# Kernel optimization log

Measured on AMD Instinct MI355X. Metric: run time of the kernel, lower is better.

The kernel has to match this reference:

```python
import jax, jax.numpy as jnp
from jax import lax
import numpy as np


def conv2d(x, w, b=None, stride=1, padding=0, groups=1, dilation=1):
    out = lax.conv_general_dilated(
        x, w, (stride, stride), [(padding, padding)] * 2,
        rhs_dilation=(dilation, dilation), feature_group_count=groups,
        dimension_numbers=('NCHW', 'OIHW', 'NCHW'))
    return out if b is None else out + b[None, :, None, None]


def unfold1d(x, k, axis):
    # torch.nn.functional.unfold with kernel (k,1) or (1,k), pad k//2 on that axis.
    # Returns [B, C, k, H, W] (channel-major, kernel-tap inner), matching torch layout.
    pad = k // 2
    pads = [(0, 0)] * 4
    pads[axis] = (pad, pad)
    xp = jnp.pad(x, pads)
    return jnp.stack([lax.slice_in_dim(xp, i, i + x.shape[axis], axis=axis)
                      for i in range(k)], axis=2)


def ikba(x, att, k, g, b_cb, w_cb):
    # Per-pixel dynamic grouped conv: attention mixes nset codebook kernels,
    # applied as vertical (k,1) then horizontal (1,k) unfold-matmul-fold.
    B, c, H, W = x.shape
    nset = att.shape[1]
    cg = c // g
    P = H * W
    a = att.reshape(B, nset, P).transpose(0, 2, 1)          # [B,P,nset]
    bias = a @ b_cb[0]                                      # [B,P,c]
    attk = a @ w_cb[0]                                      # [B,P, 2*c*cg*k]
    half = attk.shape[-1] // 2
    ah = attk[..., :half].reshape(B, P, g, cg, cg * k)
    aw = attk[..., half:].reshape(B, P, g, cg, cg * k)
    # vertical pass
    ufh = unfold1d(x, k, 2).reshape(B, g, cg * k, P).transpose(0, 3, 1, 2)  # [B,P,g,cg*k]
    xh = jnp.einsum('bpgij,bpgj->bpgi', ah, ufh).reshape(B, P, c)
    xh = xh.transpose(0, 2, 1).reshape(B, c, H, W)
    # horizontal pass
    ufw = unfold1d(xh, k, 3).reshape(B, g, cg * k, P).transpose(0, 3, 1, 2)
    xw = jnp.einsum('bpgij,bpgj->bpgi', aw, ufw).reshape(B, P, c) + bias
    return xw.transpose(0, 2, 1).reshape(B, c, H, W)


def hff_forward(x, dw1_w, dw2_w, proj_w, lka0_w, lkas_w, lka1_w, lka1_b,
                sca_w, sca_b, c1a_w, c1b_w, c2a_w, c2a_b, c2b_w, c2b_b,
                c211_w, c211_b, w_cb, b_cb, attgamma, ga1):
    C = x.shape[1]
    K, GC = 3, 4
    g = C // GC
    sca = conv2d(jnp.mean(x, axis=(2, 3), keepdims=True), sca_w, sca_b)
    x1 = conv2d(conv2d(x, dw1_w), dw2_w, padding=1, groups=C)
    lka = conv2d(conv2d(conv2d(x, lka0_w, padding=2, groups=C),
                        lkas_w, padding=9, groups=C, dilation=3), lka1_w, lka1_b)
    t = conv2d(x, c2a_w, c2a_b, padding=1, groups=c2a_w.shape[0])
    t1, t2 = jnp.split(t, 2, axis=1)  # SimpleGate
    att = conv2d(t1 * t2, c2b_w, c2b_b) * attgamma + conv2d(x, c211_w, c211_b)
    uf = conv2d(conv2d(x, c1a_w), c1b_w, padding=1, groups=C)
    x2 = ikba(uf, att, K, g, b_cb, w_cb) * ga1 + uf
    return conv2d(x1 * x2 * sca * lka, proj_w)


def setup_inputs() -> dict:
    key = jax.random.key(0)
    ks = jax.random.split(key, 24)
    B, C, H, W = 2, 256, 64, 64
    nset, k, gc = 128, 3, 4
    g = C // gc
    cg = C // g
    def rn(i, shape, scale=0.02):
        return jax.random.normal(ks[i], shape, jnp.float32) * scale
    return {
        'x': jax.random.normal(ks[0], (B, C, H, W), jnp.float32),
        'dw1_w': rn(1, (C, C, 1, 1)),
        'dw2_w': rn(2, (C, 1, 3, 3), 0.1),
        'proj_w': rn(3, (C, C, 1, 1)),
        'lka0_w': rn(4, (C, 1, 5, 5), 0.1),
        'lkas_w': rn(5, (C, 1, 7, 7), 0.1),
        'lka1_w': rn(6, (C, C, 1, 1)),
        'lka1_b': rn(7, (C,)),
        'sca_w': rn(8, (C, C, 1, 1)),
        'sca_b': rn(9, (C,)),
        'c1a_w': rn(10, (C, C, 1, 1)),
        'c1b_w': rn(11, (C, 1, 3, 3), 0.1),
        'c2a_w': rn(12, (32, C // 32, 3, 3), 0.1),
        'c2a_b': rn(13, (32,)),
        'c2b_w': rn(14, (nset, 16, 1, 1), 0.1),
        'c2b_b': rn(15, (nset,)),
        'c211_w': rn(16, (nset, C, 1, 1)),
        'c211_b': rn(17, (nset,)),
        'w_cb': rn(18, (1, nset, C * cg * k * 2), 0.05),
        'b_cb': rn(19, (1, nset, C), 0.05),
        'attgamma': jnp.full((1, nset, 1, 1), 0.01, jnp.float32),
        'ga1': jnp.full((1, C, 1, 1), 0.01, jnp.float32),
    }


def reference(x, dw1_w, dw2_w, proj_w, lka0_w, lkas_w, lka1_w, lka1_b,
              sca_w, sca_b, c1a_w, c1b_w, c2a_w, c2a_b, c2b_w, c2b_b,
              c211_w, c211_b, w_cb, b_cb, attgamma, ga1):
    return hff_forward(x, dw1_w, dw2_w, proj_w, lka0_w, lkas_w, lka1_w, lka1_b,
                       sca_w, sca_b, c1a_w, c1b_w, c2a_w, c2a_b, c2b_w, c2b_b,
                       c211_w, c211_b, w_cb, b_cb, attgamma, ga1)
```

## Files before the change

### kernel.cpp

```cpp
#include <hip/hip_runtime.h>
#include <cstddef>

#define P_ 4096
#define HW_ 64

typedef __bf16 bf16x8 __attribute__((ext_vector_type(8)));
typedef float f32x4 __attribute__((ext_vector_type(4)));

__device__ inline ushort f2bf(float f) {
  unsigned u = __float_as_uint(f);
  unsigned r = (u + 0x7FFFu + ((u >> 16) & 1u)) >> 16;
  return (ushort)r;
}
__device__ inline float bf2f(ushort h) {
  return __uint_as_float(((unsigned)h) << 16);
}
__device__ inline unsigned pack2(ushort a, ushort b) {
  return (unsigned)a | ((unsigned)b << 16);
}


__device__ inline void xsplit_body(const float* sb, ushort* dhb, ushort* dlb,
                                   int p0, int K, char* smem) {
  float (*T)[65] = (float(*)[65])smem;
  int t = threadIdx.x;
#pragma unroll
  for (int i = 0; i < 32; ++i) {
    int l = i * 256 + t;
    int n = l >> 6, c = l & 63;
    T[n][c] = sb[(size_t)n * P_ + p0 + c];
  }
  __syncthreads();
#pragma unroll
  for (int i = 0; i < 4; ++i) {
    int l = i * 256 + t;
    int c = l >> 4, n8 = (l & 15) << 3;
    ushort vh[8], vl[8];
#pragma unroll
    for (int u = 0; u < 8; ++u) {
      float f = T[n8 + u][c];
      ushort h = f2bf(f);
      vh[u] = h;
      vl[u] = f2bf(f - bf2f(h));
    }
    *(uint4*)&dhb[(size_t)(p0 + c) * K + n8] = *(uint4*)vh;
    *(uint4*)&dlb[(size_t)(p0 + c) * K + n8] = *(uint4*)vl;
  }
}

__device__ inline void gemm_body(const ushort* Whb, const ushort* Wlb,
                                 const ushort* Xhb, const ushort* Xlb,
                                 const float* bias, float* out, int M, int m0,
                                 int p0, int b, int K, char* smem) {
  ushort* Wsh = (ushort*)smem;
  ushort* Wsl = (ushort*)(smem + 9216);
  ushort* Xsh = (ushort*)(smem + 18432);
  ushort* Xsl = (ushort*)(smem + 27648);
  int t = threadIdx.x;
  int w = t >> 6, lane = t & 63, lm = lane & 15, lq = lane >> 4;
  f32x4 C[4];
#pragma unroll
  for (int pt = 0; pt < 4; ++pt) C[pt] = (f32x4)(0.f);
  for (int k0 = 0; k0 < K; k0 += 64) {
#pragma unroll
    for (int i = 0; i < 2; ++i) {
      int u = i * 256 + t;
      int row = u >> 3, k8 = (u & 7) * 8;
      *(uint4*)&Wsh[row * 72 + k8] = *(const uint4*)&Whb[(size_t)row * K + k0 + k8];
      *(uint4*)&Wsl[row * 72 + k8] = *(const uint4*)&Wlb[(size_t)row * K + k0 + k8];
      *(uint4*)&Xsh[row * 72 + k8] = *(const uint4*)&Xhb[(size_t)row * K + k0 + k8];
      *(uint4*)&Xsl[row * 72 + k8] = *(const uint4*)&Xlb[(size_t)row * K + k0 + k8];
    }
    __syncthreads();
#pragma unroll
    for (int kt = 0; kt < 2; ++kt) {
      bf16x8 Ah = *(const bf16x8*)&Wsh[(w * 16 + lm) * 72 + kt * 32 + lq * 8];
      bf16x8 Al = *(const bf16x8*)&Wsl[(w * 16 + lm) * 72 + kt * 32 + lq * 8];
#pragma unroll
      for (int pt = 0; pt < 4; ++pt) {
        bf16x8 Bh = *(const bf16x8*)&Xsh[(pt * 16 + lm) * 72 + kt * 32 + lq * 8];
        bf16x8 Bl = *(const bf16x8*)&Xsl[(pt * 16 + lm) * 72 + kt * 32 + lq * 8];
        C[pt] = __builtin_amdgcn_mfma_f32_16x16x32_bf16(Ah, Bh, C[pt], 0, 0, 0);
        C[pt] = __builtin_amdgcn_mfma_f32_16x16x32_bf16(Al, Bh, C[pt], 0, 0, 0);
        C[pt] = __builtin_amdgcn_mfma_f32_16x16x32_bf16(Ah, Bl, C[pt], 0, 0, 0);
      }
    }
    __syncthreads();
  }
#pragma unroll
  for (int pt = 0; pt < 4; ++pt) {
    int p = p0 + pt * 16 + lm;
#pragma unroll
    for (int r = 0; r < 4; ++r) {
      int m = m0 + w * 16 + lq * 4 + r;
      float v = C[pt][r];
      if (bias) v += bias[m];
      out[((size_t)b * M + m) * P_ + p] = v;
    }
  }
}

__global__ __launch_bounds__(256) void prep_kernel(
    const float* __restrict__ w_cb, const float* __restrict__ dw1_w,
    const float* __restrict__ lka1_w, const float* __restrict__ c1a_w,
    const float* __restrict__ proj_w, const float* __restrict__ c211_w,
    const float* __restrict__ b_cb, ushort* __restrict__ wT,
    ushort* __restrict__ W5h, ushort* __restrict__ W5l,
    ushort* __restrict__ bth, ushort* __restrict__ btl,
    const float* __restrict__ x, float* __restrict__ mean,
    ushort* __restrict__ XTxh, ushort* __restrict__ XTxl) {
  __shared__ __align__(16) char smem[33280];
  float (*T)[65] = (float(*)[65])smem;
  int blk = blockIdx.x;
  int t = threadIdx.x;
  if (blk < 96) {
    int c0 = blk * 64;
#pragma unroll
    for (int i = 0; i < 32; ++i) {
      int l = i * 256 + t;
      int n = l >> 6, c = l & 63;
      T[n][c] = w_cb[(size_t)n * 6144 + c0 + c];
    }
    __syncthreads();
#pragma unroll
    for (int i = 0; i < 4; ++i) {
      int l = i * 256 + t;
      int c = l >> 4, n8 = (l & 15) << 3;
      ushort v[8];
#pragma unroll
      for (int u = 0; u < 8; ++u) v[u] = f2bf(T[n8 + u][c]);
      *(uint4*)&wT[(size_t)(c0 + c) * 128 + n8] = *(uint4*)v;
    }
  } else if (blk < 240) {
    int f = (blk - 96) * 2048 + t * 8;
    const float* srcs[5] = {dw1_w, lka1_w, c1a_w, proj_w, c211_w};
    const int base[6] = {0, 65536, 131072, 196608, 262144, 294912};
    int r = 0;
    while (f >= base[r + 1]) ++r;
    const float* s = srcs[r] + (f - base[r]);
    float4 a = *(const float4*)s;
    float4 b4 = *(const float4*)(s + 4);
    float vv[8] = {a.x, a.y, a.z, a.w, b4.x, b4.y, b4.z, b4.w};
    ushort vh[8], vl[8];
#pragma unroll
    for (int u = 0; u < 8; ++u) {
      ushort h = f2bf(vv[u]);
      vh[u] = h;
      vl[u] = f2bf(vv[u] - bf2f(h));
    }
    *(uint4*)&W5h[f] = *(uint4*)vh;
    *(uint4*)&W5l[f] = *(uint4*)vl;
  } else if (blk < 244) {
    int c0 = (blk - 240) * 64;
#pragma unroll
    for (int i = 0; i < 32; ++i) {
      int l = i * 256 + t;
      int n = l >> 6, c = l & 63;
      T[n][c] = b_cb[(size_t)n * 256 + c0 + c];
    }
    __syncthreads();
#pragma unroll
    for (int i = 0; i < 4; ++i) {
      int l = i * 256 + t;
      int c = l >> 4, n8 = (l & 15) << 3;
      ushort vh[8], vl[8];
#pragma unroll
      for (int u = 0; u < 8; ++u) {
        float fv = T[n8 + u][c];
        ushort h = f2bf(fv);
        vh[u] = h;
        vl[u] = f2bf(fv - bf2f(h));
      }
      *(uint4*)&bth[(size_t)(c0 + c) * 128 + n8] = *(uint4*)vh;
      *(uint4*)&btl[(size_t)(c0 + c) * 128 + n8] = *(uint4*)vl;
    }
  } else if (blk < 756) {
    int bc = blk - 244;
    const float* xp = x + (size_t)bc * P_;
    float s = 0.f;
    for (int i = t; i < P_; i += 256) s += xp[i];
    float* red = (float*)smem;
    red[t] = s;
    __syncthreads();
    for (int off2 = 128; off2 > 0; off2 >>= 1) {
      if (t < off2) red[t] += red[t + off2];
      __syncthreads();
    }
    if (t == 0) mean[bc] = red[0] * (1.f / P_);
  } else {
    const int K = 256;
    int l = blk - 756;
    int p0 = (l & 63) * 64;
    int kb = (l >> 6) & 1;
    int b = l >> 7;
    xsplit_body(x + ((size_t)b * K + kb * 128) * P_,
                XTxh + (size_t)b * P_ * K + (size_t)kb * 128,
                XTxl + (size_t)b * P_ * K + (size_t)kb * 128, p0, K, smem);
  }
}

__global__ __launch_bounds__(256) void main1_kernel(
    const ushort* __restrict__ Xh, const ushort* __restrict__ Xl,
    const ushort* __restrict__ W5h, const ushort* __restrict__ W5l,
    const float* __restrict__ c211_b, float* __restrict__ B1,
    float* __restrict__ B3, float* __restrict__ att0,
    const float* __restrict__ x, const float* __restrict__ w0,
    const float* __restrict__ w1, float* __restrict__ outlka,
    const float* __restrict__ c2aw, const float* __restrict__ c2ab,
    float* __restrict__ sgate, const float* __restrict__ mean,
    const float* __restrict__ sca_w, const float* __restrict__ sca_b,
    float* __restrict__ sca) {
  __shared__ __align__(16) char smem[48448];
  int blk = blockIdx.x;
  int t = threadIdx.x;
  if (blk < 512) {
    float* p0a = (float*)smem;
    float* p1a = (float*)(smem + 19584);
    int bc = blk;
    const float* ib = x + (size_t)bc * P_;
    const float* wp0 = w0 + (size_t)(bc & 255) * 25;
    const float* wp1 = w1 + (size_t)(bc & 255) * 49;
    for (int i = t; i < 4896; i += 256) p0a[i] = 0.f;
    for (int i = t; i < 7216; i += 256) p1a[i] = 0.f;
    __syncthreads();
#pragma unroll
    for (int i = 0; i < 4; ++i) {
      int l = i * 1024 + t * 4;
      int y = l >> 6, xx = l & 63;
      *(float4*)&p0a[(y + 2) * 72 + 4 + xx] = *(const float4*)(ib + l);
    }
    __syncthreads();
    int x0 = (t & 15) * 4, y0 = (t >> 4) * 4;
    {
      float acc[4][4] = {};
#pragma unroll
      for (int ry = 0; ry < 8; ++ry) {
        const float* row = &p0a[(y0 + ry) * 72 + x0];
        float4 v0 = *(const float4*)row;
        float4 v1 = *(const float4*)(row + 4);
        float4 v2 = *(const float4*)(row + 8);
        float rv[12] = {v0.x, v0.y, v0.z, v0.w, v1.x, v1.y, v1.z, v1.w,
                        v2.x, v2.y, v2.z, v2.w};
#pragma unroll
        for (int oy = 0; oy < 4; ++oy) {
          int dy = ry - oy;
          if (dy >= 0 && dy <= 4) {
#pragma unroll
            for (int dx = 0; dx < 5; ++dx) {
              float wv = wp0[dy * 5 + dx];
#pragma unroll
              for (int ox = 0; ox < 4; ++ox)
                acc[oy][ox] += wv * rv[2 + ox + dx];
            }
          }
        }
      }
#pragma unroll
      for (int oy = 0; oy < 4; ++oy) {
        float4 v = {acc[oy][0], acc[oy][1], acc[oy][2], acc[oy][3]};
        *(float4*)&p1a[(y0 + oy + 9) * 88 + 12 + x0] = v;
      }
    }
    __syncthreads();
    {
      float acc[4][4] = {};
#pragma unroll
      for (int ry = 0; ry < 22; ++ry) {
        const float* row = &p1a[(y0 + ry) * 88 + x0];
        float rv[28];
#pragma unroll
        for (int q = 0; q < 7; ++q)
          *(float4*)&rv[q * 4] = *(const float4*)(row + q * 4);
#pragma unroll
        for (int oy = 0; oy < 4; ++oy) {
          int d = ry - oy;
          if (d >= 0 && d <= 18 && (d % 3) == 0) {
            int dy = d / 3;
#pragma unroll
            for (int dx = 0; dx < 7; ++dx) {
              float wv = wp1[dy * 7 + dx];
#pragma unroll
              for (int ox = 0; ox < 4; ++ox)
                acc[oy][ox] += wv * rv[3 + ox + 3 * dx];
            }
          }
        }
      }
      float* ob = outlka + (size_t)bc * P_;
#pragma unroll
      for (int oy = 0; oy < 4; ++oy) {
        float4 v = {acc[oy][0], acc[oy][1], acc[oy][2], acc[oy][3]};
        *(float4*)&ob[(y0 + oy) * 64 + x0] = v;
      }
    }
  } else if (blk < 1024) {
    int idx = (blk - 512) * 256 + t;
    int xq = idx & 63, y = (idx >> 6) & 63, go = (idx >> 12) & 15, b = idx >> 16;
    float acc[2];
#pragma unroll
    for (int h = 0; h < 2; ++h) {
      int gc = go + h * 16;
      const float* wr = c2aw + gc * 72;
      const float* xb = x + ((size_t)b * 256 + gc * 8) * P_;
      float ss = c2ab[gc];
      for (int ci = 0; ci < 8; ++ci)
        for (int dy = 0; dy < 3; ++dy) {
          int yy = y + dy - 1;
          if (yy < 0 || yy >= 64) continue;
          for (int dx = 0; dx < 3; ++dx) {
            int xx = xq + dx - 1;
            if (xx < 0 || xx >= 64) continue;
            ss += wr[ci * 9 + dy * 3 + dx] * xb[(size_t)ci * P_ + yy * 64 + xx];
          }
        }
      acc[h] = ss;
    }
    sgate[idx] = acc[0] * acc[1];
  } else if (blk < 1026) {
    int b = blk - 1024, c = t;
    const float* mb = mean + b * 256;
    const float* wr = sca_w + c * 256;
    float s = sca_b[c];
    for (int k = 0; k < 256; ++k) s += wr[k] * mb[k];
    sca[b * 256 + c] = s;
  } else {
    const int K = 256;
    int g = blk - 1026;
    int p = g & 63;
    int my = (g >> 6) % 10;
    int b = g / 640;
    const ushort *Wh, *Wl;
    float* out;
    const float* bias = nullptr;
    int M, m0;
    if (my < 4) {
      Wh = W5h; Wl = W5l; out = B1; M = 256; m0 = my * 64;
    } else if (my < 8) {
      Wh = W5h + 131072; Wl = W5l + 131072; out = B3; M = 256; m0 = (my - 4) * 64;
    } else {
      Wh = W5h + 262144; Wl = W5l + 262144; out = att0; M = 128;
      m0 = (my - 8) * 64; bias = c211_b;
    }
    int p0 = p * 64;
    gemm_body(Wh + (size_t)m0 * K, Wl + (size_t)m0 * K,
              Xh + ((size_t)b * P_ + p0) * K, Xl + ((size_t)b * P_ + p0) * K,
              bias, out, M, m0, p0, b, K, smem);
  }
}

__global__ __launch_bounds__(256) void dwsplit_kernel(
    const float* __restrict__ in1, const float* __restrict__ w1,
    float* __restrict__ out1, const float* __restrict__ in2,
    const float* __restrict__ w2, float* __restrict__ out2,
    const float* __restrict__ B6, ushort* __restrict__ XT2h,
    ushort* __restrict__ XT2l) {
  __shared__ __align__(16) char smem[33280];
  int blk = blockIdx.x;
  int t = threadIdx.x;
  if (blk < 1024) {
    float* pl = (float*)smem;
    int which = blk >> 9;
    int bc = blk & 511;
    const float* in = which ? in2 : in1;
    const float* w = which ? w2 : w1;
    float* out = which ? out2 : out1;
    const float* ib = in + (size_t)bc * P_;
    const float* wp = w + (size_t)(bc & 255) * 9;
    for (int i = t; i < 4752; i += 256) pl[i] = 0.f;
    __syncthreads();
#pragma unroll
    for (int i = 0; i < 4; ++i) {
      int l = i * 1024 + t * 4;
      int y = l >> 6, xx = l & 63;
      *(float4*)&pl[(y + 1) * 72 + 4 + xx] = *(const float4*)(ib + l);
    }
    __syncthreads();
    int x0 = (t & 15) * 4, y0 = (t >> 4) * 4;
    float acc[4][4] = {};
#pragma unroll
    for (int ry = 0; ry < 6; ++ry) {
      const float* row = &pl[(y0 + ry) * 72 + x0];
      float4 v0 = *(const float4*)row;
      float4 v1 = *(const float4*)(row + 4);
      float4 v2 = *(const float4*)(row + 8);
      float rv[12] = {v0.x, v0.y, v0.z, v0.w, v1.x, v1.y, v1.z, v1.w,
                      v2.x, v2.y, v2.z, v2.w};
#pragma unroll
      for (int oy = 0; oy < 4; ++oy) {
        int dy = ry - oy;
        if (dy >= 0 && dy <= 2) {
#pragma unroll
          for (int dx = 0; dx < 3; ++dx) {
            float wv = wp[dy * 3 + dx];
#pragma unroll
            for (int ox = 0; ox < 4; ++ox)
              acc[oy][ox] += wv * rv[3 + ox + dx];
          }
        }
      }
    }
    float* ob = out + (size_t)bc * P_;
#pragma unroll
    for (int oy = 0; oy < 4; ++oy) {
      float4 v = {acc[oy][0], acc[oy][1], acc[oy][2], acc[oy][3]};
      *(float4*)&ob[(y0 + oy) * 64 + x0] = v;
    }
  } else {
    const int K = 256;
    int l = blk - 1024;
    int p0 = (l & 63) * 64;
    int kb = (l >> 6) & 1;
    int b = l >> 7;
    xsplit_body(B6 + ((size_t)b * K + kb * 128) * P_,
                XT2h + (size_t)b * P_ * K + (size_t)kb * 128,
                XT2l + (size_t)b * P_ * K + (size_t)kb * 128, p0, K, smem);
  }
}

__global__ __launch_bounds__(256) void gemm_c2b_kernel(
    const ushort* __restrict__ Wh, const ushort* __restrict__ Wl,
    const ushort* __restrict__ XT2h, const ushort* __restrict__ XT2l,
    const float* __restrict__ lka1_b, float* __restrict__ B1,
    const float* __restrict__ sb, const float* __restrict__ c2bw,
    const float* __restrict__ c2bb, const float* __restrict__ gamma,
    const float* __restrict__ res, ushort* __restrict__ outh,
    ushort* __restrict__ outl) {
  __shared__ __align__(16) char smem[36864];
  int my = blockIdx.y;
  int b = blockIdx.z;
  int t = threadIdx.x;
  if (my < 4) {
    const int K = 256;
    int p0 = blockIdx.x * 64, m0 = my * 64;
    gemm_body(Wh + (size_t)m0 * K, Wl + (size_t)m0 * K,
              XT2h + ((size_t)b * P_ + p0) * K, XT2l + ((size_t)b * P_ + p0) * K,
              lka1_b, B1, 256, m0, p0, b, K, smem);
  } else {
    const int K = 16, M = 128;
    int p0 = blockIdx.x * 64;
    int m0 = (my - 4) * 64;
    float (*Ws)[68] = (float(*)[68])smem;
    float (*Xs)[68] = (float(*)[68])(smem + 4352 * 4);
    int tm = t >> 4, tp = t & 15;
    float acc[4][4] = {};
    const float* inb = sb + (size_t)b * K * P_;
    {
      int kk = t >> 4, pq = (t & 15) << 2;
      float4 v = *(const float4*)(inb + (size_t)kk * P_ + p0 + pq);
      *(float4*)&Xs[kk][pq] = v;
    }
    {
      int mm = t >> 2, kq = (t & 3) << 2;
      float4 v = *(const float4*)(c2bw + (size_t)(m0 + mm) * K + kq);
      Ws[kq + 0][mm] = v.x; Ws[kq + 1][mm] = v.y;
      Ws[kq + 2][mm] = v.z; Ws[kq + 3][mm] = v.w;
    }
    __syncthreads();
#pragma unroll
    for (int kk = 0; kk < 16; ++kk) {
      const float4 wv = *(const float4*)&Ws[kk][tm << 2];
      const float4 xv = *(const float4*)&Xs[kk][tp << 2];
      const float wa[4] = {wv.x, wv.y, wv.z, wv.w};
      const float xa[4] = {xv.x, xv.y, xv.z, xv.w};
#pragma unroll
      for (int i = 0; i < 4; ++i)
#pragma unroll
        for (int j = 0; j < 4; ++j) acc[i][j] += wa[i] * xa[j];
    }
    float val[4][4];
#pragma unroll
    for (int i = 0; i < 4; ++i) {
      int m = m0 + (tm << 2) + i;
      float bv = c2bb[m], gm = gamma[m];
      float4 rv = *(const float4*)(res + ((size_t)b * M + m) * P_ + p0 + (tp << 2));
      val[i][0] = (acc[i][0] + bv) * gm + rv.x;
      val[i][1] = (acc[i][1] + bv) * gm + rv.y;
      val[i][2] = (acc[i][2] + bv) * gm + rv.z;
      val[i][3] = (acc[i][3] + bv) * gm + rv.w;
    }
#pragma unroll
    for (int j = 0; j < 4; ++j) {
      int p = p0 + (tp << 2) + j;
      ushort vh[4], vl[4];
#pragma unroll
      for (int i = 0; i < 4; ++i) {
        float f = val[i][j];
        ushort h = f2bf(f);
        vh[i] = h;
        vl[i] = f2bf(f - bf2f(h));
      }
      size_t a = ((size_t)b * P_ + p) * 128 + m0 + (tm << 2);
      uint2 hv, lv;
      hv.x = pack2(vh[0], vh[1]); hv.y = pack2(vh[2], vh[3]);
      lv.x = pack2(vl[0], vl[1]); lv.y = pack2(vl[2], vl[3]);
      *(uint2*)&outh[a] = hv;
      *(uint2*)&outl[a] = lv;
    }
  }
}

__global__ __launch_bounds__(256) void ikba_mfma_kernel(
    const float* __restrict__ in, const ushort* __restrict__ attT,
    const ushort* __restrict__ Wt, int dirH, int wofs,
    const ushort* __restrict__ bth, const ushort* __restrict__ btl,
    const float* __restrict__ uf_ep, const float* __restrict__ ga1,
    const float* __restrict__ x1, const float* __restrict__ lka,
    const float* __restrict__ sca, ushort* __restrict__ pXh,
    ushort* __restrict__ pXl, float* __restrict__ outV) {
  __shared__ float Ts[2][4][16][66];
  __shared__ float bls[64 * 17];

  int t = threadIdx.x;
  int b = blockIdx.z;
  int quad = blockIdx.y;
  int y = blockIdx.x;
  int p0 = y * 64;
  int gg = t >> 6;
  int lane = t & 63;
  int lm = lane & 15, lq = lane >> 4;
  int gi = quad * 4 + gg;
  int x = lane;

  const ushort* Wbase = Wt + ((size_t)wofs + (size_t)gi * 48) * 128;
  bf16x8 Af[3][4];
#pragma unroll
  for (int ct = 0; ct < 3; ++ct)
#pragma unroll
    for (int K = 0; K < 4; ++K)
      Af[ct][K] = *(const bf16x8*)&Wbase[(ct * 16 + lm) * 128 + K * 32 + lq * 8];

  const ushort* Ab = attT + ((size_t)b * P_ + p0) * 128;
  f32x4 Cf[3][4];
#pragma unroll
  for (int ct = 0; ct < 3; ++ct)
#pragma unroll
    for (int pt = 0; pt < 4; ++pt) Cf[ct][pt] = (f32x4)(0.f);

#pragma unroll
  for (int pt = 0; pt < 4; ++pt) {
    bf16x8 Bf[4];
#pragma unroll
    for (int K = 0; K < 4; ++K)
      Bf[K] = *(const bf16x8*)&Ab[(pt * 16 + lm) * 128 + K * 32 + lq * 8];
#pragma unroll
    for (int ct = 0; ct < 3; ++ct)
#pragma unroll
      for (int K = 0; K < 4; ++K)
        Cf[ct][pt] = __builtin_amdgcn_mfma_f32_16x16x32_bf16(
            Af[ct][K], Bf[K], Cf[ct][pt], 0, 0, 0);
  }

  if (dirH) {
    f32x4 Cb = (f32x4)(0.f);
#pragma unroll
    for (int K = 0; K < 4; ++K) {
      bf16x8 Bb = *(const bf16x8*)&Ab[(gg * 16 + lm) * 128 + K * 32 + lq * 8];
      bf16x8 Abh = *(const bf16x8*)&bth[(size_t)(quad * 16 + lm) * 128 + K * 32 + lq * 8];
      bf16x8 Abl = *(const bf16x8*)&btl[(size_t)(quad * 16 + lm) * 128 + K * 32 + lq * 8];
      Cb = __builtin_amdgcn_mfma_f32_16x16x32_bf16(Abh, Bb, Cb, 0, 0, 0);
      Cb = __builtin_amdgcn_mfma_f32_16x16x32_bf16(Abl, Bb, Cb, 0, 0, 0);
    }
#pragma unroll
    for (int r = 0; r < 4; ++r)
      bls[(gg * 16 + lm) * 17 + lq * 4 + r] = Cb[r];
  }

  float u[12];
  const float* inb = in + ((size_t)b * 256 + gi * 4) * P_;
  if (dirH) {
#pragma unroll
    for (int j = 0; j < 12; ++j) {
      int ci = j / 3, tap = j % 3;
      int xx = x + tap - 1;
      u[j] = (xx >= 0 && xx < 64) ? inb[(size_t)ci * P_ + p0 + xx] : 0.f;
    }
  } else {
#pragma unroll
    for (int j = 0; j < 12; ++j) {
      int ci = j / 3, tap = j % 3;
      int yy = y + tap - 1;
      u[j] = (yy >= 0 && yy < 64) ? inb[(size_t)ci * P_ + yy * 64 + x] : 0.f;
    }
  }

  float s4[4] = {0.f, 0.f, 0.f, 0.f};
#pragma unroll
  for (int ct = 0; ct < 3; ++ct) {
    int bi = ct & 1;
#pragma unroll
    for (int pt = 0; pt < 4; ++pt)
#pragma unroll
      for (int r = 0; r < 4; ++r)
        Ts[bi][gg][lq * 4 + r][pt * 16 + lm] = Cf[ct][pt][r];
    __syncthreads();
#pragma unroll
    for (int cl = 0; cl < 16; ++cl) {
      int col = ct * 16 + cl;
      int i = col / 12, j = col % 12;
      s4[i] += Ts[bi][gg][cl][x] * u[j];
    }
  }

#pragma unroll
  for (int i = 0; i < 4; ++i) {
    int ch = gi * 4 + i;
    size_t oidx = ((size_t)b * 256 + ch) * P_ + p0 + x;
    if (dirH) {
      float biasv = bls[x * 17 + gg * 4 + i];
      float x2v = (s4[i] + biasv) * ga1[ch] + uf_ep[oidx];
      float pr = x1[oidx] * x2v * sca[b * 256 + ch] * lka[oidx];
      ushort h = f2bf(pr);
      ushort lo = f2bf(pr - bf2f(h));
      s4[i] = __uint_as_float(pack2(h, lo));
    } else {
      outV[oidx] = s4[i];
    }
  }
  if (dirH) {
    size_t xa = ((size_t)b * P_ + p0 + x) * 256 + quad * 16 + gg * 4;
    uint2 hv, lv;
    unsigned w0 = __float_as_uint(s4[0]), w1 = __float_as_uint(s4[1]);
    unsigned w2 = __float_as_uint(s4[2]), w3 = __float_as_uint(s4[3]);
    hv.x = (w0 & 0xFFFFu) | ((w1 & 0xFFFFu) << 16);
    hv.y = (w2 & 0xFFFFu) | ((w3 & 0xFFFFu) << 16);
    lv.x = (w0 >> 16) | (w1 & 0xFFFF0000u);
    lv.y = (w2 >> 16) | (w3 & 0xFFFF0000u);
    *(uint2*)&pXh[xa] = hv;
    *(uint2*)&pXl[xa] = lv;
  }
}

__global__ __launch_bounds__(256) void gemm_bf16s_kernel(
    const ushort* __restrict__ Wh, const ushort* __restrict__ Wl,
    const ushort* __restrict__ Xh, const ushort* __restrict__ Xl,
    const float* __restrict__ bias, float* __restrict__ out, int M, int K) {
  __shared__ __align__(16) char smem[36864];
  int p0 = blockIdx.x * 64, m0 = blockIdx.y * 64, b = blockIdx.z;
  gemm_body(Wh + (size_t)m0 * K, Wl + (size_t)m0 * K,
            Xh + ((size_t)b * P_ + p0) * K, Xl + ((size_t)b * P_ + p0) * K,
            bias, out, M, m0, p0, b, K, smem);
}

extern "C" void kernel_launch(void* const* d_in, const int* in_sizes, int n_in,
                              void* d_out, int out_size, void* d_ws, size_t ws_size,
                              hipStream_t stream) {
  const float* x      = (const float*)d_in[0];
  const float* dw1_w  = (const float*)d_in[1];
  const float* dw2_w  = (const float*)d_in[2];
  const float* proj_w = (const float*)d_in[3];
  const float* lka0_w = (const float*)d_in[4];
  const float* lkas_w = (const float*)d_in[5];
  const float* lka1_w = (const float*)d_in[6];
  const float* lka1_b = (const float*)d_in[7];
  const float* sca_w  = (const float*)d_in[8];
  const float* sca_b  = (const float*)d_in[9];
  const float* c1a_w  = (const float*)d_in[10];
  const float* c1b_w  = (const float*)d_in[11];
  const float* c2a_w  = (const float*)d_in[12];
  const float* c2a_b  = (const float*)d_in[13];
  const float* c2b_w  = (const float*)d_in[14];
  const float* c2b_b  = (const float*)d_in[15];
  const float* c211_w = (const float*)d_in[16];
  const float* c211_b = (const float*)d_in[17];
  const float* w_cb   = (const float*)d_in[18];
  const float* b_cb   = (const float*)d_in[19];
  const float* attg   = (const float*)d_in[20];
  const float* ga1    = (const float*)d_in[21];
  float* out = (float*)d_out;

  const size_t NCHW = 2u * 256u * P_;
  float* ws = (float*)d_ws;
  size_t off = 0;
  float* meanb = ws + off; off += 512;
  float* scab  = ws + off; off += 512;
  float* B1 = ws + off; off += NCHW;
  float* B2 = ws + off; off += NCHW;
  float* B3 = ws + off; off += NCHW;
  float* B4 = ws + off; off += NCHW;
  float* B5 = ws + off; off += NCHW;
  float* B6 = ws + off; off += NCHW;
  float* sb   = ws + off; off += 2u * 16u * P_;
  float* att0 = ws + off; off += 2u * 128u * P_;
  ushort* wT    = (ushort*)(ws + off); off += 393216;
  ushort* W5h   = (ushort*)(ws + off); off += 147456;
  ushort* W5l   = (ushort*)(ws + off); off += 147456;
  ushort* bth   = (ushort*)(ws + off); off += 16384;
  ushort* btl   = (ushort*)(ws + off); off += 16384;
  ushort* XTxh  = (ushort*)(ws + off); off += 1048576;
  ushort* XTxl  = (ushort*)(ws + off); off += 1048576;
  ushort* XT2h  = (ushort*)(ws + off); off += 1048576;
  ushort* XT2l  = (ushort*)(ws + off); off += 1048576;
  ushort* XT3h  = (ushort*)(ws + off); off += 1048576;
  ushort* XT3l  = (ushort*)(ws + off); off += 1048576;
  ushort* attTh = (ushort*)(ws + off); off += 524288;
  ushort* attTl = (ushort*)(ws + off); off += 524288;

  const ushort* Wlka1h = W5h + 65536,  *Wlka1l = W5l + 65536;
  const ushort* Wprojh = W5h + 196608, *Wprojl = W5l + 196608;

  dim3 blk(256);

  prep_kernel<<<1012, blk, 0, stream>>>(w_cb, dw1_w, lka1_w, c1a_w, proj_w,
                                        c211_w, b_cb, wT, W5h, W5l, bth, btl,
                                        x, meanb, XTxh, XTxl);
  main1_kernel<<<2306, blk, 0, stream>>>(XTxh, XTxl, W5h, W5l, c211_b,
                                         B1, B3, att0, x, lka0_w, lkas_w, B6,
                                         c2a_w, c2a_b, sb, meanb, sca_w, sca_b,
                                         scab);
  dwsplit_kernel<<<1280, blk, 0, stream>>>(B1, dw2_w, B2, B3, c1b_w, B5,
                                           B6, XT2h, XT2l);
  gemm_c2b_kernel<<<dim3(64, 6, 2), blk, 0, stream>>>(
      Wlka1h, Wlka1l, XT2h, XT2l, lka1_b, B1,
      sb, c2b_w, c2b_b, attg, att0, attTh, attTl);
  dim3 gik(64, 16, 2);
  ikba_mfma_kernel<<<gik, blk, 0, stream>>>(B5, attTh, wT, 0, 0, nullptr, nullptr,
                                            nullptr, nullptr, nullptr, nullptr,
                                            nullptr, nullptr, nullptr, B4);
  ikba_mfma_kernel<<<gik, blk, 0, stream>>>(B4, attTh, wT, 1, 3072, bth, btl,
                                            B5, ga1, B2, B1, scab, XT3h, XT3l,
                                            nullptr);
  gemm_bf16s_kernel<<<dim3(64, 4, 2), blk, 0, stream>>>(Wprojh, Wprojl, XT3h,
                                                        XT3l, nullptr, out, 256, 256);
}
```

Baseline: 266.6 us.

## Prefetch next GEMM K-tile into registers and repad depthwise conv LDS rows

The split-bf16 GEMM body now loads the next 64-wide K slice of W and X into registers while the MFMAs on the current slice run, then writes them to LDS at the start of the next iteration. This hides global load latency behind compute at the cost of extra VGPRs. Separately, the LDS row strides of the depthwise 5x5/7x7 and 3x3 conv tiles grow from 72/88 to 76/92 floats to reduce bank conflicts on the float4 row reads. The LDS allocation and zero-fill sizes are enlarged to match.

```diff
diff --git a/kernel.cpp b/kernel.cpp
--- a/kernel.cpp
+++ b/kernel.cpp
@@ -58,20 +58,40 @@
   ushort* Xsl = (ushort*)(smem + 27648);
   int t = threadIdx.x;
   int w = t >> 6, lane = t & 63, lm = lane & 15, lq = lane >> 4;
+  int row = t >> 3, k8 = (t & 7) * 8;
   f32x4 C[4];
 #pragma unroll
   for (int pt = 0; pt < 4; ++pt) C[pt] = (f32x4)(0.f);
+  uint4 pw_h[2], pw_l[2], px_h[2], px_l[2];
+#pragma unroll
+  for (int i = 0; i < 2; ++i) {
+    int r2 = i * 32 + row;
+    pw_h[i] = *(const uint4*)&Whb[(size_t)r2 * K + k8];
+    pw_l[i] = *(const uint4*)&Wlb[(size_t)r2 * K + k8];
+    px_h[i] = *(const uint4*)&Xhb[(size_t)r2 * K + k8];
+    px_l[i] = *(const uint4*)&Xlb[(size_t)r2 * K + k8];
+  }
   for (int k0 = 0; k0 < K; k0 += 64) {
 #pragma unroll
     for (int i = 0; i < 2; ++i) {
-      int u = i * 256 + t;
-      int row = u >> 3, k8 = (u & 7) * 8;
-      *(uint4*)&Wsh[row * 72 + k8] = *(const uint4*)&Whb[(size_t)row * K + k0 + k8];
-      *(uint4*)&Wsl[row * 72 + k8] = *(const uint4*)&Wlb[(size_t)row * K + k0 + k8];
-      *(uint4*)&Xsh[row * 72 + k8] = *(const uint4*)&Xhb[(size_t)row * K + k0 + k8];
-      *(uint4*)&Xsl[row * 72 + k8] = *(const uint4*)&Xlb[(size_t)row * K + k0 + k8];
-    }
-    __syncthreads();
+      int r2 = i * 32 + row;
+      *(uint4*)&Wsh[r2 * 72 + k8] = pw_h[i];
+      *(uint4*)&Wsl[r2 * 72 + k8] = pw_l[i];
+      *(uint4*)&Xsh[r2 * 72 + k8] = px_h[i];
+      *(uint4*)&Xsl[r2 * 72 + k8] = px_l[i];
+    }
+    __syncthreads();
+    if (k0 + 64 < K) {
+      int kn = k0 + 64;
+#pragma unroll
+      for (int i = 0; i < 2; ++i) {
+        int r2 = i * 32 + row;
+        pw_h[i] = *(const uint4*)&Whb[(size_t)r2 * K + kn + k8];
+        pw_l[i] = *(const uint4*)&Wlb[(size_t)r2 * K + kn + k8];
+        px_h[i] = *(const uint4*)&Xhb[(size_t)r2 * K + kn + k8];
+        px_l[i] = *(const uint4*)&Xlb[(size_t)r2 * K + kn + k8];
+      }
+    }
 #pragma unroll
     for (int kt = 0; kt < 2; ++kt) {
       bf16x8 Ah = *(const bf16x8*)&Wsh[(w * 16 + lm) * 72 + kt * 32 + lq * 8];
@@ -210,24 +230,24 @@
     float* __restrict__ sgate, const float* __restrict__ mean,
     const float* __restrict__ sca_w, const float* __restrict__ sca_b,
     float* __restrict__ sca) {
-  __shared__ __align__(16) char smem[48448];
+  __shared__ __align__(16) char smem[50848];
   int blk = blockIdx.x;
   int t = threadIdx.x;
   if (blk < 512) {
     float* p0a = (float*)smem;
-    float* p1a = (float*)(smem + 19584);
+    float* p1a = (float*)(smem + 20672);
     int bc = blk;
     const float* ib = x + (size_t)bc * P_;
     const float* wp0 = w0 + (size_t)(bc & 255) * 25;
     const float* wp1 = w1 + (size_t)(bc & 255) * 49;
-    for (int i = t; i < 4896; i += 256) p0a[i] = 0.f;
-    for (int i = t; i < 7216; i += 256) p1a[i] = 0.f;
+    for (int i = t; i < 5168; i += 256) p0a[i] = 0.f;
+    for (int i = t; i < 7544; i += 256) p1a[i] = 0.f;
     __syncthreads();
 #pragma unroll
     for (int i = 0; i < 4; ++i) {
       int l = i * 1024 + t * 4;
       int y = l >> 6, xx = l & 63;
-      *(float4*)&p0a[(y + 2) * 72 + 4 + xx] = *(const float4*)(ib + l);
+      *(float4*)&p0a[(y + 2) * 76 + 4 + xx] = *(const float4*)(ib + l);
     }
     __syncthreads();
     int x0 = (t & 15) * 4, y0 = (t >> 4) * 4;
@@ -235,7 +255,7 @@
       float acc[4][4] = {};
 #pragma unroll
       for (int ry = 0; ry < 8; ++ry) {
-        const float* row = &p0a[(y0 + ry) * 72 + x0];
+        const float* row = &p0a[(y0 + ry) * 76 + x0];
         float4 v0 = *(const float4*)row;
         float4 v1 = *(const float4*)(row + 4);
         float4 v2 = *(const float4*)(row + 8);
@@ -258,7 +278,7 @@
 #pragma unroll
       for (int oy = 0; oy < 4; ++oy) {
         float4 v = {acc[oy][0], acc[oy][1], acc[oy][2], acc[oy][3]};
-        *(float4*)&p1a[(y0 + oy + 9) * 88 + 12 + x0] = v;
+        *(float4*)&p1a[(y0 + oy + 9) * 92 + 12 + x0] = v;
       }
     }
     __syncthreads();
@@ -266,7 +286,7 @@
       float acc[4][4] = {};
 #pragma unroll
       for (int ry = 0; ry < 22; ++ry) {
-        const float* row = &p1a[(y0 + ry) * 88 + x0];
+        const float* row = &p1a[(y0 + ry) * 92 + x0];
         float rv[28];
 #pragma unroll
         for (int q = 0; q < 7; ++q)
@@ -366,20 +386,20 @@
     float* out = which ? out2 : out1;
     const float* ib = in + (size_t)bc * P_;
     const float* wp = w + (size_t)(bc & 255) * 9;
-    for (int i = t; i < 4752; i += 256) pl[i] = 0.f;
+    for (int i = t; i < 5016; i += 256) pl[i] = 0.f;
     __syncthreads();
 #pragma unroll
     for (int i = 0; i < 4; ++i) {
       int l = i * 1024 + t * 4;
       int y = l >> 6, xx = l & 63;
-      *(float4*)&pl[(y + 1) * 72 + 4 + xx] = *(const float4*)(ib + l);
+      *(float4*)&pl[(y + 1) * 76 + 4 + xx] = *(const float4*)(ib + l);
     }
     __syncthreads();
     int x0 = (t & 15) * 4, y0 = (t >> 4) * 4;
     float acc[4][4] = {};
 #pragma unroll
     for (int ry = 0; ry < 6; ++ry) {
-      const float* row = &pl[(y0 + ry) * 72 + x0];
+      const float* row = &pl[(y0 + ry) * 76 + x0];
       float4 v0 = *(const float4*)row;
       float4 v1 = *(const float4*)(row + 4);
       float4 v2 = *(const float4*)(row + 8);
```

Result: slower. 333.0 us (+24.9%).

## Rebalance kernel stages to merge dwsplit into neighbors and cut a launch

Applied to the files above, without the earlier changes.

Reschedules work across launches: the LKA depthwise conv moves into the prep kernel, the B6 transpose-split and the SCA matvec move into main1 next to the 1x1 GEMMs, and the 3x3 depthwise convs merge with the lka1/c2b GEMMs in a new k3 kernel. This removes one kernel launch and its barrier, and lets independent tasks share a grid so they overlap. Buffers are reassigned (B4/B6 reused) to respect the new dependencies. In exchange, the grids mix heterogeneous block types, and prep's larger shared-memory footprint may lower occupancy.

```diff
diff --git a/kernel.cpp b/kernel.cpp
--- a/kernel.cpp
+++ b/kernel.cpp
@@ -108,109 +108,11 @@
     ushort* __restrict__ W5h, ushort* __restrict__ W5l,
     ushort* __restrict__ bth, ushort* __restrict__ btl,
     const float* __restrict__ x, float* __restrict__ mean,
-    ushort* __restrict__ XTxh, ushort* __restrict__ XTxl) {
-  __shared__ __align__(16) char smem[33280];
+    ushort* __restrict__ XTxh, ushort* __restrict__ XTxl,
+    const float* __restrict__ w0, const float* __restrict__ w1,
+    float* __restrict__ outlka) {
+  __shared__ __align__(16) char smem[48448];
   float (*T)[65] = (float(*)[65])smem;
-  int blk = blockIdx.x;
-  int t = threadIdx.x;
-  if (blk < 96) {
-    int c0 = blk * 64;
-#pragma unroll
-    for (int i = 0; i < 32; ++i) {
-      int l = i * 256 + t;
-      int n = l >> 6, c = l & 63;
-      T[n][c] = w_cb[(size_t)n * 6144 + c0 + c];
-    }
-    __syncthreads();
-#pragma unroll
-    for (int i = 0; i < 4; ++i) {
-      int l = i * 256 + t;
-      int c = l >> 4, n8 = (l & 15) << 3;
-      ushort v[8];
-#pragma unroll
-      for (int u = 0; u < 8; ++u) v[u] = f2bf(T[n8 + u][c]);
-      *(uint4*)&wT[(size_t)(c0 + c) * 128 + n8] = *(uint4*)v;
-    }
-  } else if (blk < 240) {
-    int f = (blk - 96) * 2048 + t * 8;
-    const float* srcs[5] = {dw1_w, lka1_w, c1a_w, proj_w, c211_w};
-    const int base[6] = {0, 65536, 131072, 196608, 262144, 294912};
-    int r = 0;
-    while (f >= base[r + 1]) ++r;
-    const float* s = srcs[r] + (f - base[r]);
-    float4 a = *(const float4*)s;
-    float4 b4 = *(const float4*)(s + 4);
-    float vv[8] = {a.x, a.y, a.z, a.w, b4.x, b4.y, b4.z, b4.w};
-    ushort vh[8], vl[8];
-#pragma unroll
-    for (int u = 0; u < 8; ++u) {
-      ushort h = f2bf(vv[u]);
-      vh[u] = h;
-      vl[u] = f2bf(vv[u] - bf2f(h));
-    }
-    *(uint4*)&W5h[f] = *(uint4*)vh;
-    *(uint4*)&W5l[f] = *(uint4*)vl;
-  } else if (blk < 244) {
-    int c0 = (blk - 240) * 64;
-#pragma unroll
-    for (int i = 0; i < 32; ++i) {
-      int l = i * 256 + t;
-      int n = l >> 6, c = l & 63;
-      T[n][c] = b_cb[(size_t)n * 256 + c0 + c];
-    }
-    __syncthreads();
-#pragma unroll
-    for (int i = 0; i < 4; ++i) {
-      int l = i * 256 + t;
-      int c = l >> 4, n8 = (l & 15) << 3;
-      ushort vh[8], vl[8];
-#pragma unroll
-      for (int u = 0; u < 8; ++u) {
-        float fv = T[n8 + u][c];
-        ushort h = f2bf(fv);
-        vh[u] = h;
-        vl[u] = f2bf(fv - bf2f(h));
-      }
-      *(uint4*)&bth[(size_t)(c0 + c) * 128 + n8] = *(uint4*)vh;
-      *(uint4*)&btl[(size_t)(c0 + c) * 128 + n8] = *(uint4*)vl;
-    }
-  } else if (blk < 756) {
-    int bc = blk - 244;
-    const float* xp = x + (size_t)bc * P_;
-    float s = 0.f;
-    for (int i = t; i < P_; i += 256) s += xp[i];
-    float* red = (float*)smem;
-    red[t] = s;
-    __syncthreads();
-    for (int off2 = 128; off2 > 0; off2 >>= 1) {
-      if (t < off2) red[t] += red[t + off2];
-      __syncthreads();
-    }
-    if (t == 0) mean[bc] = red[0] * (1.f / P_);
-  } else {
-    const int K = 256;
-    int l = blk - 756;
-    int p0 = (l & 63) * 64;
-    int kb = (l >> 6) & 1;
-    int b = l >> 7;
-    xsplit_body(x + ((size_t)b * K + kb * 128) * P_,
-                XTxh + (size_t)b * P_ * K + (size_t)kb * 128,
-                XTxl + (size_t)b * P_ * K + (size_t)kb * 128, p0, K, smem);
-  }
-}
-
-__global__ __launch_bounds__(256) void main1_kernel(
-    const ushort* __restrict__ Xh, const ushort* __restrict__ Xl,
-    const ushort* __restrict__ W5h, const ushort* __restrict__ W5l,
-    const float* __restrict__ c211_b, float* __restrict__ B1,
-    float* __restrict__ B3, float* __restrict__ att0,
-    const float* __restrict__ x, const float* __restrict__ w0,
-    const float* __restrict__ w1, float* __restrict__ outlka,
-    const float* __restrict__ c2aw, const float* __restrict__ c2ab,
-    float* __restrict__ sgate, const float* __restrict__ mean,
-    const float* __restrict__ sca_w, const float* __restrict__ sca_b,
-    float* __restrict__ sca) {
-  __shared__ __align__(16) char smem[48448];
   int blk = blockIdx.x;
   int t = threadIdx.x;
   if (blk < 512) {
@@ -293,8 +195,129 @@
         *(float4*)&ob[(y0 + oy) * 64 + x0] = v;
       }
     }
-  } else if (blk < 1024) {
-    int idx = (blk - 512) * 256 + t;
+  } else if (blk < 608) {
+    int c0 = (blk - 512) * 64;
+#pragma unroll
+    for (int i = 0; i < 32; ++i) {
+      int l = i * 256 + t;
+      int n = l >> 6, c = l & 63;
+      T[n][c] = w_cb[(size_t)n * 6144 + c0 + c];
+    }
+    __syncthreads();
+#pragma unroll
+    for (int i = 0; i < 4; ++i) {
+      int l = i * 256 + t;
+      int c = l >> 4, n8 = (l & 15) << 3;
+      ushort v[8];
+#pragma unroll
+      for (int u = 0; u < 8; ++u) v[u] = f2bf(T[n8 + u][c]);
+      *(uint4*)&wT[(size_t)(c0 + c) * 128 + n8] = *(uint4*)v;
+    }
+  } else if (blk < 752) {
+    int f = (blk - 608) * 2048 + t * 8;
+    const float* srcs[5] = {dw1_w, lka1_w, c1a_w, proj_w, c211_w};
+    const int base[6] = {0, 65536, 131072, 196608, 262144, 294912};
+    int r = 0;
+    while (f >= base[r + 1]) ++r;
+    const float* s = srcs[r] + (f - base[r]);
+    float4 a = *(const float4*)s;
+    float4 b4 = *(const float4*)(s + 4);
+    float vv[8] = {a.x, a.y, a.z, a.w, b4.x, b4.y, b4.z, b4.w};
+    ushort vh[8], vl[8];
+#pragma unroll
+    for (int u = 0; u < 8; ++u) {
+      ushort h = f2bf(vv[u]);
+      vh[u] = h;
+      vl[u] = f2bf(vv[u] - bf2f(h));
+    }
+    *(uint4*)&W5h[f] = *(uint4*)vh;
+    *(uint4*)&W5l[f] = *(uint4*)vl;
+  } else if (blk < 756) {
+    int c0 = (blk - 752) * 64;
+#pragma unroll
+    for (int i = 0; i < 32; ++i) {
+      int l = i * 256 + t;
+      int n = l >> 6, c = l & 63;
+      T[n][c] = b_cb[(size_t)n * 256 + c0 + c];
+    }
+    __syncthreads();
+#pragma unroll
+    for (int i = 0; i < 4; ++i) {
+      int l = i * 256 + t;
+      int c = l >> 4, n8 = (l & 15) << 3;
+      ushort vh[8], vl[8];
+#pragma unroll
+      for (int u = 0; u < 8; ++u) {
+        float fv = T[n8 + u][c];
+        ushort h = f2bf(fv);
+        vh[u] = h;
+        vl[u] = f2bf(fv - bf2f(h));
+      }
+      *(uint4*)&bth[(size_t)(c0 + c) * 128 + n8] = *(uint4*)vh;
+      *(uint4*)&btl[(size_t)(c0 + c) * 128 + n8] = *(uint4*)vl;
+    }
+  } else if (blk < 1268) {
+    int bc = blk - 756;
+    const float* xp = x + (size_t)bc * P_;
+    float s = 0.f;
+    for (int i = t; i < P_; i += 256) s += xp[i];
+    float* red = (float*)smem;
+    red[t] = s;
+    __syncthreads();
+    for (int off2 = 128; off2 > 0; off2 >>= 1) {
+      if (t < off2) red[t] += red[t + off2];
+      __syncthreads();
+    }
+    if (t == 0) mean[bc] = red[0] * (1.f / P_);
+  } else {
+    const int K = 256;
+    int l = blk - 1268;
+    int p0 = (l & 63) * 64;
+    int kb = (l >> 6) & 1;
+    int b = l >> 7;
+    xsplit_body(x + ((size_t)b * K + kb * 128) * P_,
+                XTxh + (size_t)b * P_ * K + (size_t)kb * 128,
+                XTxl + (size_t)b * P_ * K + (size_t)kb * 128, p0, K, smem);
+  }
+}
+
+__global__ __launch_bounds__(256) void main1_kernel(
+    const ushort* __restrict__ Xh, const ushort* __restrict__ Xl,
+    const ushort* __restrict__ W5h, const ushort* __restrict__ W5l,
+    const float* __restrict__ c211_b, float* __restrict__ dw1_out,
+    float* __restrict__ B3, float* __restrict__ att0,
+    const float* __restrict__ x, const float* __restrict__ c2aw,
+    const float* __restrict__ c2ab, float* __restrict__ sgate,
+    const float* __restrict__ B6, ushort* __restrict__ XT2h,
+    ushort* __restrict__ XT2l, const float* __restrict__ mean,
+    const float* __restrict__ sca_w, const float* __restrict__ sca_b,
+    float* __restrict__ sca) {
+  __shared__ __align__(16) char smem[36864];
+  int blk = blockIdx.x;
+  int t = threadIdx.x;
+  if (blk < 1280) {
+    const int K = 256;
+    int p = blk & 63;
+    int my = (blk >> 6) % 10;
+    int b = blk / 640;
+    const ushort *Wh, *Wl;
+    float* out;
+    const float* bias = nullptr;
+    int M, m0;
+    if (my < 4) {
+      Wh = W5h; Wl = W5l; out = dw1_out; M = 256; m0 = my * 64;
+    } else if (my < 8) {
+      Wh = W5h + 131072; Wl = W5l + 131072; out = B3; M = 256; m0 = (my - 4) * 64;
+    } else {
+      Wh = W5h + 262144; Wl = W5l + 262144; out = att0; M = 128;
+      m0 = (my - 8) * 64; bias = c211_b;
+    }
+    int p0 = p * 64;
+    gemm_body(Wh + (size_t)m0 * K, Wl + (size_t)m0 * K,
+              Xh + ((size_t)b * P_ + p0) * K, Xl + ((size_t)b * P_ + p0) * K,
+              bias, out, M, m0, p0, b, K, smem);
+  } else if (blk < 1792) {
+    int idx = (blk - 1280) * 256 + t;
     int xq = idx & 63, y = (idx >> 6) & 63, go = (idx >> 12) & 15, b = idx >> 16;
     float acc[2];
 #pragma unroll
@@ -316,129 +339,53 @@
       acc[h] = ss;
     }
     sgate[idx] = acc[0] * acc[1];
-  } else if (blk < 1026) {
-    int b = blk - 1024, c = t;
-    const float* mb = mean + b * 256;
-    const float* wr = sca_w + c * 256;
-    float s = sca_b[c];
-    for (int k = 0; k < 256; ++k) s += wr[k] * mb[k];
-    sca[b * 256 + c] = s;
-  } else {
+  } else if (blk < 2048) {
     const int K = 256;
-    int g = blk - 1026;
-    int p = g & 63;
-    int my = (g >> 6) % 10;
-    int b = g / 640;
-    const ushort *Wh, *Wl;
-    float* out;
-    const float* bias = nullptr;
-    int M, m0;
-    if (my < 4) {
-      Wh = W5h; Wl = W5l; out = B1; M = 256; m0 = my * 64;
-    } else if (my < 8) {
-      Wh = W5h + 131072; Wl = W5l + 131072; out = B3; M = 256; m0 = (my - 4) * 64;
-    } else {
-      Wh = W5h + 262144; Wl = W5l + 262144; out = att0; M = 128;
-      m0 = (my - 8) * 64; bias = c211_b;
-    }
-    int p0 = p * 64;
-    gemm_body(Wh + (size_t)m0 * K, Wl + (size_t)m0 * K,
-              Xh + ((size_t)b * P_ + p0) * K, Xl + ((size_t)b * P_ + p0) * K,
-              bias, out, M, m0, p0, b, K, smem);
-  }
-}
-
-__global__ __launch_bounds__(256) void dwsplit_kernel(
-    const float* __restrict__ in1, const float* __restrict__ w1,
-    float* __restrict__ out1, const float* __restrict__ in2,
-    const float* __restrict__ w2, float* __restrict__ out2,
-    const float* __restrict__ B6, ushort* __restrict__ XT2h,
-    ushort* __restrict__ XT2l) {
-  __shared__ __align__(16) char smem[33280];
-  int blk = blockIdx.x;
-  int t = threadIdx.x;
-  if (blk < 1024) {
-    float* pl = (float*)smem;
-    int which = blk >> 9;
-    int bc = blk & 511;
-    const float* in = which ? in2 : in1;
-    const float* w = which ? w2 : w1;
-    float* out = which ? out2 : out1;
-    const float* ib = in + (size_t)bc * P_;
-    const float* wp = w + (size_t)(bc & 255) * 9;
-    for (int i = t; i < 4752; i += 256) pl[i] = 0.f;
-    __syncthreads();
-#pragma unroll
-    for (int i = 0; i < 4; ++i) {
-      int l = i * 1024 + t * 4;
-      int y = l >> 6, xx = l & 63;
-      *(float4*)&pl[(y + 1) * 72 + 4 + xx] = *(const float4*)(ib + l);
-    }
-    __syncthreads();
-    int x0 = (t & 15) * 4, y0 = (t >> 4) * 4;
-    float acc[4][4] = {};
-#pragma unroll
-    for (int ry = 0; ry < 6; ++ry) {
-      const float* row = &pl[(y0 + ry) * 72 + x0];
-      float4 v0 = *(const float4*)row;
-      float4 v1 = *(const float4*)(row + 4);
-      float4 v2 = *(const float4*)(row + 8);
-      float rv[12] = {v0.x, v0.y, v0.z, v0.w, v1.x, v1.y, v1.z, v1.w,
-                      v2.x, v2.y, v2.z, v2.w};
-#pragma unroll
-      for (int oy = 0; oy < 4; ++oy) {
-        int dy = ry - oy;
-        if (dy >= 0 && dy <= 2) {
-#pragma unroll
-          for (int dx = 0; dx < 3; ++dx) {
-            float wv = wp[dy * 3 + dx];
-#pragma unroll
-            for (int ox = 0; ox < 4; ++ox)
-              acc[oy][ox] += wv * rv[3 + ox + dx];
-          }
-        }
-      }
-    }
-    float* ob = out + (size_t)bc * P_;
-#pragma unroll
-    for (int oy = 0; oy < 4; ++oy) {
-      float4 v = {acc[oy][0], acc[oy][1], acc[oy][2], acc[oy][3]};
-      *(float4*)&ob[(y0 + oy) * 64 + x0] = v;
-    }
-  } else {
-    const int K = 256;
-    int l = blk - 1024;
+    int l = blk - 1792;
     int p0 = (l & 63) * 64;
     int kb = (l >> 6) & 1;
     int b = l >> 7;
     xsplit_body(B6 + ((size_t)b * K + kb * 128) * P_,
                 XT2h + (size_t)b * P_ * K + (size_t)kb * 128,
                 XT2l + (size_t)b * P_ * K + (size_t)kb * 128, p0, K, smem);
-  }
-}
-
-__global__ __launch_bounds__(256) void gemm_c2b_kernel(
+  } else {
+    int b = blk - 2048, c = t;
+    const float* mb = mean + b * 256;
+    const float* wr = sca_w + c * 256;
+    float s = sca_b[c];
+    for (int k = 0; k < 256; ++k) s += wr[k] * mb[k];
+    sca[b * 256 + c] = s;
+  }
+}
+
+__global__ __launch_bounds__(256) void k3_kernel(
     const ushort* __restrict__ Wh, const ushort* __restrict__ Wl,
     const ushort* __restrict__ XT2h, const ushort* __restrict__ XT2l,
     const float* __restrict__ lka1_b, float* __restrict__ B1,
     const float* __restrict__ sb, const float* __restrict__ c2bw,
     const float* __restrict__ c2bb, const float* __restrict__ gamma,
     const float* __restrict__ res, ushort* __restrict__ outh,
-    ushort* __restrict__ outl) {
+    ushort* __restrict__ outl, const float* __restrict__ in1,
+    const float* __restrict__ w1, float* __restrict__ out1,
+    const float* __restrict__ in2, const float* __restrict__ w2,
+    float* __restrict__ out2) {
   __shared__ __align__(16) char smem[36864];
-  int my = blockIdx.y;
-  int b = blockIdx.z;
+  int blk = blockIdx.x;
   int t = threadIdx.x;
-  if (my < 4) {
+  if (blk < 512) {
     const int K = 256;
-    int p0 = blockIdx.x * 64, m0 = my * 64;
+    int p0 = (blk & 63) * 64;
+    int m0 = ((blk >> 6) & 3) * 64;
+    int b = blk >> 8;
     gemm_body(Wh + (size_t)m0 * K, Wl + (size_t)m0 * K,
               XT2h + ((size_t)b * P_ + p0) * K, XT2l + ((size_t)b * P_ + p0) * K,
               lka1_b, B1, 256, m0, p0, b, K, smem);
-  } else {
+  } else if (blk < 768) {
     const int K = 16, M = 128;
-    int p0 = blockIdx.x * 64;
-    int m0 = (my - 4) * 64;
+    int l = blk - 512;
+    int p0 = (l & 63) * 64;
+    int m0 = ((l >> 6) & 1) * 64;
+    int b = l >> 7;
     float (*Ws)[68] = (float(*)[68])smem;
     float (*Xs)[68] = (float(*)[68])(smem + 4352 * 4);
     int tm = t >> 4, tp = t & 15;
@@ -495,6 +442,55 @@
       lv.x = pack2(vl[0], vl[1]); lv.y = pack2(vl[2], vl[3]);
       *(uint2*)&outh[a] = hv;
       *(uint2*)&outl[a] = lv;
+    }
+  } else {
+    float* pl = (float*)smem;
+    int l = blk - 768;
+    int which = l >> 9;
+    int bc = l & 511;
+    const float* in = which ? in2 : in1;
+    const float* w = which ? w2 : w1;
+    float* out = which ? out2 : out1;
+    const float* ib = in + (size_t)bc * P_;
+    const float* wp = w + (size_t)(bc & 255) * 9;
+    for (int i = t; i < 4752; i += 256) pl[i] = 0.f;
+    __syncthreads();
+#pragma unroll
+    for (int i = 0; i < 4; ++i) {
+      int ll = i * 1024 + t * 4;
+      int y = ll >> 6, xx = ll & 63;
+      *(float4*)&pl[(y + 1) * 72 + 4 + xx] = *(const float4*)(ib + ll);
+    }
+    __syncthreads();
+    int x0 = (t & 15) * 4, y0 = (t >> 4) * 4;
+    float acc[4][4] = {};
+#pragma unroll
+    for (int ry = 0; ry < 6; ++ry) {
+      const float* row = &pl[(y0 + ry) * 72 + x0];
+      float4 v0 = *(const float4*)row;
+      float4 v1 = *(const float4*)(row + 4);
+      float4 v2 = *(const float4*)(row + 8);
+      float rv[12] = {v0.x, v0.y, v0.z, v0.w, v1.x, v1.y, v1.z, v1.w,
+                      v2.x, v2.y, v2.z, v2.w};
+#pragma unroll
+      for (int oy = 0; oy < 4; ++oy) {
+        int dy = ry - oy;
+        if (dy >= 0 && dy <= 2) {
+#pragma unroll
+          for (int dx = 0; dx < 3; ++dx) {
+            float wv = wp[dy * 3 + dx];
+#pragma unroll
+            for (int ox = 0; ox < 4; ++ox)
+              acc[oy][ox] += wv * rv[3 + ox + dx];
+          }
+        }
+      }
+    }
+    float* ob = out + (size_t)bc * P_;
+#pragma unroll
+    for (int oy = 0; oy < 4; ++oy) {
+      float4 v = {acc[oy][0], acc[oy][1], acc[oy][2], acc[oy][3]};
+      *(float4*)&ob[(y0 + oy) * 64 + x0] = v;
     }
   }
 }
@@ -700,23 +696,23 @@
 
   dim3 blk(256);
 
-  prep_kernel<<<1012, blk, 0, stream>>>(w_cb, dw1_w, lka1_w, c1a_w, proj_w,
+  prep_kernel<<<1524, blk, 0, stream>>>(w_cb, dw1_w, lka1_w, c1a_w, proj_w,
                                         c211_w, b_cb, wT, W5h, W5l, bth, btl,
-                                        x, meanb, XTxh, XTxl);
-  main1_kernel<<<2306, blk, 0, stream>>>(XTxh, XTxl, W5h, W5l, c211_b,
-                                         B1, B3, att0, x, lka0_w, lkas_w, B6,
-                                         c2a_w, c2a_b, sb, meanb, sca_w, sca_b,
+                                        x, meanb, XTxh, XTxl,
+                                        lka0_w, lkas_w, B6);
+  main1_kernel<<<2050, blk, 0, stream>>>(XTxh, XTxl, W5h, W5l, c211_b,
+                                         B4, B3, att0, x, c2a_w, c2a_b, sb,
+                                         B6, XT2h, XT2l, meanb, sca_w, sca_b,
                                          scab);
-  dwsplit_kernel<<<1280, blk, 0, stream>>>(B1, dw2_w, B2, B3, c1b_w, B5,
-                                           B6, XT2h, XT2l);
-  gemm_c2b_kernel<<<dim3(64, 6, 2), blk, 0, stream>>>(
-      Wlka1h, Wlka1l, XT2h, XT2l, lka1_b, B1,
-      sb, c2b_w, c2b_b, attg, att0, attTh, attTl);
+  k3_kernel<<<1792, blk, 0, stream>>>(Wlka1h, Wlka1l, XT2h, XT2l, lka1_b, B1,
+                                      sb, c2b_w, c2b_b, attg, att0,
+                                      attTh, attTl,
+                                      B4, dw2_w, B2, B3, c1b_w, B5);
   dim3 gik(64, 16, 2);
   ikba_mfma_kernel<<<gik, blk, 0, stream>>>(B5, attTh, wT, 0, 0, nullptr, nullptr,
                                             nullptr, nullptr, nullptr, nullptr,
-                                            nullptr, nullptr, nullptr, B4);
-  ikba_mfma_kernel<<<gik, blk, 0, stream>>>(B4, attTh, wT, 1, 3072, bth, btl,
+                                            nullptr, nullptr, nullptr, B6);
+  ikba_mfma_kernel<<<gik, blk, 0, stream>>>(B6, attTh, wT, 1, 3072, bth, btl,
                                             B5, ga1, B2, B1, scab, XT3h, XT3l,
                                             nullptr);
   gemm_bf16s_kernel<<<dim3(64, 4, 2), blk, 0, stream>>>(Wprojh, Wprojl, XT3h,
```

Result: no change. 264.3 us (-0.8%).
